# Performance work log

Hardware: AMD Instinct MI355X
Metric: run time of the kernel (lower is better)

## Reference

```python
import jax, jax.numpy as jnp
import numpy as np

N, D, O = 131072, 128, 256

def setup_inputs() -> dict:
    key = jax.random.key(0)
    k1, k2, k3 = jax.random.split(key, 3)
    return {
        "targets": jax.random.normal(k1, (N, 1), dtype=jnp.float32),
        "out0": jnp.zeros((1,), dtype=jnp.float32),
        "out1": jnp.zeros((1,), dtype=jnp.float32),
        "graph_emb": jax.random.normal(k2, (N, D), dtype=jnp.float32),
        "errors": jax.random.normal(k3, (N, O), dtype=jnp.float32),
    }

def reference(targets, out0, out1, graph_emb, errors):
    # errors: [N, O]; graph_emb: [N, D]. Original nested loop computes
    # cov[i,o] = (errors[i,o]-mean_o) * (graph_emb[i,0]-mean_emb[0]),
    # cov_error = sum_o | sum_i cov[i,o] |; returns -cov_error.
    errors_minus_mean = errors - jnp.mean(errors, axis=0)            # [N, O]
    act_minus_mean = graph_emb - jnp.mean(graph_emb, axis=0)         # [N, D]
    a0 = act_minus_mean[:, :1]                                       # [N, 1] (only col 0 used)
    col_sums = jnp.sum(errors_minus_mean * a0, axis=0)               # [O]
    cov_error = jnp.sum(jnp.abs(col_sums))
    return -cov_error
```

## Files before the change

kernel.cpp:

```cpp
#include <hip/hip_runtime.h>


#define NB 1024
#define BT 512

__global__ __launch_bounds__(BT) void cov_main_kernel(
    const float* __restrict__ errors,
    const float* __restrict__ graph_emb,
    float* __restrict__ partials,
    int N, int D, int O)
{
    const int tid = threadIdx.x;
    const int g   = tid >> 6;
    const int l   = tid & 63;
    const int vecPerRow = O >> 2;

    const float4* __restrict__ err4 = (const float4*)errors;

    float a0 = 0.f, a1 = 0.f, a2 = 0.f, a3 = 0.f;
    float b0 = 0.f, b1 = 0.f, b2 = 0.f, b3 = 0.f;
    float gsum = 0.f;

    const int nRG = N >> 3;
    #pragma unroll 4
    for (int rg = blockIdx.x; rg < nRG; rg += NB) {
        const int row = (rg << 3) + g;
        const float gv = graph_emb[row * D];
        const float4 e = err4[row * vecPerRow + l];
        a0 = fmaf(e.x, gv, a0);
        a1 = fmaf(e.y, gv, a1);
        a2 = fmaf(e.z, gv, a2);
        a3 = fmaf(e.w, gv, a3);
        b0 += e.x; b1 += e.y; b2 += e.z; b3 += e.w;
        if (l == 0) gsum += gv;
    }

    __shared__ float sA[4 * BT];
    __shared__ float sB[4 * BT];
    __shared__ float sG[8];
    sA[0 * BT + tid] = a0; sA[1 * BT + tid] = a1;
    sA[2 * BT + tid] = a2; sA[3 * BT + tid] = a3;
    sB[0 * BT + tid] = b0; sB[1 * BT + tid] = b1;
    sB[2 * BT + tid] = b2; sB[3 * BT + tid] = b3;
    if (l == 0) sG[g] = gsum;
    __syncthreads();

    if (tid < 64) {
        float ra0 = 0.f, ra1 = 0.f, ra2 = 0.f, ra3 = 0.f;
        float rb0 = 0.f, rb1 = 0.f, rb2 = 0.f, rb3 = 0.f;
        #pragma unroll
        for (int gg = 0; gg < 8; ++gg) {
            const int idx = gg * 64 + tid;
            ra0 += sA[0 * BT + idx]; ra1 += sA[1 * BT + idx];
            ra2 += sA[2 * BT + idx]; ra3 += sA[3 * BT + idx];
            rb0 += sB[0 * BT + idx]; rb1 += sB[1 * BT + idx];
            rb2 += sB[2 * BT + idx]; rb3 += sB[3 * BT + idx];
        }
        const int b = blockIdx.x;
        const int c = tid * 4;
        partials[(c + 0) * NB + b] = ra0;
        partials[(c + 1) * NB + b] = ra1;
        partials[(c + 2) * NB + b] = ra2;
        partials[(c + 3) * NB + b] = ra3;
        partials[(256 + c + 0) * NB + b] = rb0;
        partials[(256 + c + 1) * NB + b] = rb1;
        partials[(256 + c + 2) * NB + b] = rb2;
        partials[(256 + c + 3) * NB + b] = rb3;
    }
    if (tid == 0) {
        float s = 0.f;
        #pragma unroll
        for (int gg = 0; gg < 8; ++gg) s += sG[gg];
        partials[512 * NB + blockIdx.x] = s;
    }
}

__global__ __launch_bounds__(256) void cov_reduce_kernel(
    const float* __restrict__ partials, float* __restrict__ acc)
{
    const int c = blockIdx.x;
    const int tid = threadIdx.x;
    const float4 p = ((const float4*)(partials + c * NB))[tid];
    float v = p.x + p.y + p.z + p.w;
    #pragma unroll
    for (int off = 32; off > 0; off >>= 1)
        v += __shfl_down(v, off, 64);
    __shared__ float sW[4];
    if ((tid & 63) == 0) sW[tid >> 6] = v;
    __syncthreads();
    if (tid == 0) acc[c] = sW[0] + sW[1] + sW[2] + sW[3];
}

__global__ __launch_bounds__(256) void cov_final_kernel(
    const float* __restrict__ acc, float* __restrict__ out, int N, int O)
{
    const int tid = threadIdx.x;
    const float mu = acc[512] / (float)N;
    float v = 0.f;
    if (tid < O) {
        const float cs = acc[tid] - mu * acc[256 + tid];
        v = fabsf(cs);
    }
    #pragma unroll
    for (int off = 32; off > 0; off >>= 1)
        v += __shfl_down(v, off, 64);
    __shared__ float sW[4];
    if ((tid & 63) == 0) sW[tid >> 6] = v;
    __syncthreads();
    if (tid == 0) out[0] = -(sW[0] + sW[1] + sW[2] + sW[3]);
}

extern "C" void kernel_launch(void* const* d_in, const int* in_sizes, int n_in,
                              void* d_out, int out_size, void* d_ws, size_t ws_size,
                              hipStream_t stream) {
    const int N = in_sizes[0];
    const int D = in_sizes[3] / N;
    const int O = in_sizes[4] / N;
    const float* graph_emb = (const float*)d_in[3];
    const float* errors    = (const float*)d_in[4];

    float* partials = (float*)d_ws;
    float* acc      = partials + 513 * NB;

    cov_main_kernel<<<NB, BT, 0, stream>>>(errors, graph_emb, partials, N, D, O);
    cov_reduce_kernel<<<513, 256, 0, stream>>>(partials, acc);
    cov_final_kernel<<<1, 256, 0, stream>>>(acc, (float*)d_out, N, O);
}
```

Baseline: 240.2 us.

## Store per-block partials row-major and restructure reduction into two-level tree

The main kernel now gives each block a contiguous chunk of rows instead of a grid-strided set, and raises the unroll factor. Each block writes its 513 partial sums as one padded row using coalesced float4 stores, replacing the earlier column-major layout that scattered single-float writes across memory. The 513-block reduce kernel becomes 32 blocks that each sum 32 partial rows with float2 loads. The final kernel then sums those 32 rows. This aims to cut the uncoalesced store traffic and the launch overhead of the reduction, at the cost of less parallelism in the middle reduction stage.

```diff
diff --git a/kernel.cpp b/kernel.cpp
--- a/kernel.cpp
+++ b/kernel.cpp
@@ -3,6 +3,7 @@
 
 #define NB 1024
 #define BT 512
+#define RPAD 516
 
 __global__ __launch_bounds__(BT) void cov_main_kernel(
     const float* __restrict__ errors,
@@ -19,12 +20,15 @@
 
     float a0 = 0.f, a1 = 0.f, a2 = 0.f, a3 = 0.f;
     float b0 = 0.f, b1 = 0.f, b2 = 0.f, b3 = 0.f;
-    float gsum = 0.f;
+    float gs = 0.f;
 
-    const int nRG = N >> 3;
-    #pragma unroll 4
-    for (int rg = blockIdx.x; rg < nRG; rg += NB) {
-        const int row = (rg << 3) + g;
+    const int rowsPerBlock = N / NB;
+    const int iters = rowsPerBlock >> 3;
+    const int base = blockIdx.x * rowsPerBlock;
+
+    #pragma unroll 8
+    for (int it = 0; it < iters; ++it) {
+        const int row = base + (it << 3) + g;
         const float gv = graph_emb[row * D];
         const float4 e = err4[row * vecPerRow + l];
         a0 = fmaf(e.x, gv, a0);
@@ -32,7 +36,7 @@
         a2 = fmaf(e.z, gv, a2);
         a3 = fmaf(e.w, gv, a3);
         b0 += e.x; b1 += e.y; b2 += e.z; b3 += e.w;
-        if (l == 0) gsum += gv;
+        gs += gv;
     }
 
     __shared__ float sA[4 * BT];
@@ -42,9 +46,10 @@
     sA[2 * BT + tid] = a2; sA[3 * BT + tid] = a3;
     sB[0 * BT + tid] = b0; sB[1 * BT + tid] = b1;
     sB[2 * BT + tid] = b2; sB[3 * BT + tid] = b3;
-    if (l == 0) sG[g] = gsum;
+    if (l == 0) sG[g] = gs;
     __syncthreads();
 
+    float* __restrict__ rowp = partials + (size_t)blockIdx.x * RPAD;
     if (tid < 64) {
         float ra0 = 0.f, ra1 = 0.f, ra2 = 0.f, ra3 = 0.f;
         float rb0 = 0.f, rb1 = 0.f, rb2 = 0.f, rb3 = 0.f;
@@ -56,51 +61,56 @@
             rb0 += sB[0 * BT + idx]; rb1 += sB[1 * BT + idx];
             rb2 += sB[2 * BT + idx]; rb3 += sB[3 * BT + idx];
         }
-        const int b = blockIdx.x;
-        const int c = tid * 4;
-        partials[(c + 0) * NB + b] = ra0;
-        partials[(c + 1) * NB + b] = ra1;
-        partials[(c + 2) * NB + b] = ra2;
-        partials[(c + 3) * NB + b] = ra3;
-        partials[(256 + c + 0) * NB + b] = rb0;
-        partials[(256 + c + 1) * NB + b] = rb1;
-        partials[(256 + c + 2) * NB + b] = rb2;
-        partials[(256 + c + 3) * NB + b] = rb3;
+        ((float4*)rowp)[tid]       = make_float4(ra0, ra1, ra2, ra3);
+        ((float4*)(rowp + 256))[tid] = make_float4(rb0, rb1, rb2, rb3);
     }
     if (tid == 0) {
-        float s = 0.f;
-        #pragma unroll
-        for (int gg = 0; gg < 8; ++gg) s += sG[gg];
-        partials[512 * NB + blockIdx.x] = s;
+        rowp[512] = sG[0] + sG[1] + sG[2] + sG[3] +
+                    sG[4] + sG[5] + sG[6] + sG[7];
     }
 }
 
 __global__ __launch_bounds__(256) void cov_reduce_kernel(
-    const float* __restrict__ partials, float* __restrict__ acc)
+    const float* __restrict__ partials,
+    float* __restrict__ partial2)
 {
-    const int c = blockIdx.x;
     const int tid = threadIdx.x;
-    const float4 p = ((const float4*)(partials + c * NB))[tid];
-    float v = p.x + p.y + p.z + p.w;
-    #pragma unroll
-    for (int off = 32; off > 0; off >>= 1)
-        v += __shfl_down(v, off, 64);
-    __shared__ float sW[4];
-    if ((tid & 63) == 0) sW[tid >> 6] = v;
-    __syncthreads();
-    if (tid == 0) acc[c] = sW[0] + sW[1] + sW[2] + sW[3];
+    const int k = blockIdx.x;
+    const int rowsPer = NB / 32;
+    const int rbase = k * rowsPer;
+    float sx = 0.f, sy = 0.f, sg = 0.f;
+    for (int r = 0; r < rowsPer; ++r) {
+        const float* rowp = partials + (size_t)(rbase + r) * RPAD;
+        const float2 v = ((const float2*)rowp)[tid];
+        sx += v.x; sy += v.y;
+        sg += rowp[512];
+    }
+    float* orow = partial2 + (size_t)k * RPAD;
+    ((float2*)orow)[tid] = make_float2(sx, sy);
+    if (tid == 0) orow[512] = sg;
 }
 
 __global__ __launch_bounds__(256) void cov_final_kernel(
-    const float* __restrict__ acc, float* __restrict__ out, int N, int O)
+    const float* __restrict__ partial2,
+    float* __restrict__ out, int N)
 {
     const int tid = threadIdx.x;
-    const float mu = acc[512] / (float)N;
-    float v = 0.f;
-    if (tid < O) {
-        const float cs = acc[tid] - mu * acc[256 + tid];
-        v = fabsf(cs);
+    float sx = 0.f, sy = 0.f, sg = 0.f;
+    #pragma unroll
+    for (int r = 0; r < 32; ++r) {
+        const float* rowp = partial2 + (size_t)r * RPAD;
+        const float2 v = ((const float2*)rowp)[tid];
+        sx += v.x; sy += v.y;
+        sg += rowp[512];
     }
+    __shared__ float sCol[513];
+    sCol[2 * tid]     = sx;
+    sCol[2 * tid + 1] = sy;
+    if (tid == 0) sCol[512] = sg;
+    __syncthreads();
+
+    const float mu = sCol[512] / (float)N;
+    float v = fabsf(sCol[tid] - mu * sCol[256 + tid]);
     #pragma unroll
     for (int off = 32; off > 0; off >>= 1)
         v += __shfl_down(v, off, 64);
@@ -120,9 +130,9 @@
     const float* errors    = (const float*)d_in[4];
 
     float* partials = (float*)d_ws;
-    float* acc      = partials + 513 * NB;
+    float* partial2 = partials + (size_t)NB * RPAD;
 
     cov_main_kernel<<<NB, BT, 0, stream>>>(errors, graph_emb, partials, N, D, O);
-    cov_reduce_kernel<<<513, 256, 0, stream>>>(partials, acc);
-    cov_final_kernel<<<1, 256, 0, stream>>>(acc, (float*)d_out, N, O);
+    cov_reduce_kernel<<<32, 256, 0, stream>>>(partials, partial2);
+    cov_final_kernel<<<1, 256, 0, stream>>>(partial2, (float*)d_out, N);
 }
```

Measured after the change: 240.6 us. Within noise of the previous version (+0.1%).
